# Kernel optimization log

Hardware: AMD Instinct MI355X
Metric: run time of the kernel (lower is better)

## Reference

```python
import jax, jax.numpy as jnp
import numpy as np
import math

B, T, N, DIN, DOUT, K, ED, H = 16, 12, 2048, 1, 64, 3, 10, 4
HORIZON, ODIM = 12, 1


def _pos_encoding(L, d, dtype):
    pos = jnp.arange(L, dtype=dtype)[:, None]
    div = jnp.exp(jnp.arange(0, d, 2, dtype=dtype) * (-math.log(10000.0) / d))
    pe = jnp.zeros((L, d), dtype)
    pe = pe.at[:, 0::2].set(jnp.sin(pos * div))
    pe = pe.at[:, 1::2].set(jnp.cos(pos * div))
    return pe  # [L, d]


def _cheb_supports(emb, cheb_k):
    # adaptive adjacency from node embeddings + Chebyshev polynomials
    A = jax.nn.softmax(jax.nn.relu(emb @ emb.T), axis=1)  # [N, N]
    supports = [jnp.eye(emb.shape[0], dtype=emb.dtype), A]
    for _ in range(2, cheb_k):
        supports.append(2.0 * (A @ supports[-1]) - supports[-2])
    return jnp.stack(supports[:cheb_k], axis=0)  # [K, N, N]


def _forward(source, targets, node_embeddings, gate_w, gate_b, update_w, update_b,
             attn_in_w, attn_in_b, attn_out_w, attn_out_b, channel_w, conv_w, conv_b):
    supports = _cheb_supports(node_embeddings, K)  # [K, N, N]
    # per-node adaptive weights (hoisted out of the time loop: constant per step)
    gw = jnp.einsum('nd,dkio->nkio', node_embeddings, gate_w)    # [N,K,DIN+DOUT,2*DOUT]
    gb = node_embeddings @ gate_b                                 # [N,2*DOUT]
    uw = jnp.einsum('nd,dkio->nkio', node_embeddings, update_w)  # [N,K,DIN+DOUT,DOUT]
    ub = node_embeddings @ update_b                               # [N,DOUT]

    def gconv(x, w, b):  # x: [B,N,C]
        xg = jnp.einsum('knm,bmc->bnkc', supports, x)
        return jnp.einsum('bnki,nkio->bno', xg, w) + b

    def gru(x, h):  # AGCRN GRU cell with adaptive graph conv
        ih = jnp.concatenate([x, h], axis=-1)
        zr = jax.nn.sigmoid(gconv(ih, gw, gb))
        z, r = zr[..., :DOUT], zr[..., DOUT:]
        hc = jnp.tanh(gconv(jnp.concatenate([x, z * h], axis=-1), uw, ub))
        return r * h + (1.0 - r) * hc

    h0 = jnp.zeros((B, N, DOUT), source.dtype)

    def step(carry, xt):
        s, ls = carry
        s2, ls2 = gru(xt, s), gru(xt, ls)
        return (s2, ls2), (s2, ls2)

    xs = jnp.swapaxes(source, 0, 1)  # [T,B,N,DIN]
    _, (states, last_states) = jax.lax.scan(step, (h0, h0), xs)
    states = jnp.swapaxes(states, 0, 1)            # [B,T,N,DOUT]
    last_states = jnp.swapaxes(last_states, 0, 1)  # [B,T,N,DOUT]

    # TransformerLayer applied to pass-1 states (eval: dropout is identity)
    def transformer(X):
        Bx, Tx, Nx, E = X.shape
        Xf = jnp.swapaxes(X, 0, 1).reshape(Tx, Bx * Nx, E)
        Xf = Xf + _pos_encoding(Tx, E, X.dtype)[:, None, :]
        qkv = Xf @ attn_in_w.T + attn_in_b
        q, k, v = jnp.split(qkv, 3, axis=-1)
        hd = E // H
        q = q.reshape(Tx, Bx * Nx, H, hd)
        k = k.reshape(Tx, Bx * Nx, H, hd)
        v = v.reshape(Tx, Bx * Nx, H, hd)
        scores = jnp.einsum('tmhd,smhd->mhts', q, k) / jnp.sqrt(jnp.asarray(hd, X.dtype))
        attn = jax.nn.softmax(scores, axis=-1)
        out = jnp.einsum('mhts,smhd->tmhd', attn, v).reshape(Tx, Bx * Nx, E)
        out = out @ attn_out_w.T + attn_out_b
        return jnp.swapaxes(out.reshape(Tx, Bx, Nx, E), 0, 1)

    current_inputs = transformer(states)   # pass 1 (with transformer)
    current_inputs_short = states          # pass 2 recomputes identical recurrence
    current_last_inputs = last_states

    o1 = current_inputs[:, -1]        # [B,N,DOUT]
    o2 = current_last_inputs[:, -1]
    o3 = current_inputs_short[:, -1]
    feat = jnp.stack([o1, o2, o3], axis=1)            # [B,3,N,DOUT]
    feat = feat * channel_w[None, :, None, None]
    out = jnp.einsum('bcnh,och->bon', feat, conv_w) + conv_b[None, :, None]  # [B,H*O,N]
    out = out.reshape(B, HORIZON, ODIM, N).transpose(0, 1, 3, 2)             # [B,H,N,O]
    return out


def setup_inputs() -> dict:
    key = jax.random.key(0)
    ks = jax.random.split(key, 10)
    s = 0.05
    return dict(
        source=jax.random.normal(ks[0], (B, T, N, DIN), jnp.float32),
        targets=jax.random.normal(ks[1], (B, HORIZON, N, ODIM), jnp.float32),
        node_embeddings=jax.random.normal(ks[2], (N, ED), jnp.float32),
        gate_w=jax.random.normal(ks[3], (ED, K, DIN + DOUT, 2 * DOUT), jnp.float32) * s,
        gate_b=jax.random.normal(ks[4], (ED, 2 * DOUT), jnp.float32) * s,
        update_w=jax.random.normal(ks[5], (ED, K, DIN + DOUT, DOUT), jnp.float32) * s,
        update_b=jax.random.normal(ks[6], (ED, DOUT), jnp.float32) * s,
        attn_in_w=jax.random.normal(ks[7], (3 * DOUT, DOUT), jnp.float32) * s,
        attn_in_b=jnp.zeros((3 * DOUT,), jnp.float32),
        attn_out_w=jax.random.normal(ks[8], (DOUT, DOUT), jnp.float32) * s,
        attn_out_b=jnp.zeros((DOUT,), jnp.float32),
        channel_w=jnp.ones((3,), jnp.float32),
        conv_w=jax.random.normal(ks[9], (HORIZON * ODIM, 3, DOUT), jnp.float32) * s,
        conv_b=jnp.zeros((HORIZON * ODIM,), jnp.float32),
    )


def reference(source, targets, node_embeddings, gate_w, gate_b, update_w, update_b,
              attn_in_w, attn_in_b, attn_out_w, attn_out_b, channel_w, conv_w, conv_b):
    return _forward(source, targets, node_embeddings, gate_w, gate_b, update_w, update_b,
                    attn_in_w, attn_in_b, attn_out_w, attn_out_b, channel_w, conv_w, conv_b)
```

## Files before the change

kernel.cpp:

```cpp
#include <hip/hip_runtime.h>
#include <hip/hip_bf16.h>

typedef _Float16 f16x8 __attribute__((ext_vector_type(8)));
typedef _Float16 f16x4 __attribute__((ext_vector_type(4)));
typedef float f32x4 __attribute__((ext_vector_type(4)));
typedef unsigned short us8 __attribute__((ext_vector_type(8)));
typedef unsigned short us4 __attribute__((ext_vector_type(4)));

#define N_ 2048
#define B_ 16
#define T_ 12
#define DH 64
#define CC 65
#define NC 1040
#define NCP 1088
#define KI 195
#define NKC 25
#define EDIM 10
#define ASCALE 1024.0f
#define AINV (1.0f / 1024.0f)

__global__ __launch_bounds__(256) void k_compA(const float* __restrict__ emb,
                                               _Float16* __restrict__ A) {
    int n = blockIdx.x, tid = threadIdx.x;
    float en[EDIM];
#pragma unroll
    for (int d = 0; d < EDIM; ++d) en[d] = emb[n * EDIM + d];
    float v[8], mx = -1e30f;
#pragma unroll
    for (int j = 0; j < 8; ++j) {
        int m = tid + j * 256;
        float acc = 0.f;
#pragma unroll
        for (int d = 0; d < EDIM; ++d) acc = fmaf(en[d], emb[m * EDIM + d], acc);
        acc = fmaxf(acc, 0.f);
        v[j] = acc; mx = fmaxf(mx, acc);
    }
    __shared__ float red[256];
    red[tid] = mx; __syncthreads();
    for (int s = 128; s > 0; s >>= 1) { if (tid < s) red[tid] = fmaxf(red[tid], red[tid + s]); __syncthreads(); }
    mx = red[0]; __syncthreads();
    float se = 0.f;
#pragma unroll
    for (int j = 0; j < 8; ++j) { v[j] = __expf(v[j] - mx); se += v[j]; }
    red[tid] = se; __syncthreads();
    for (int s = 128; s > 0; s >>= 1) { if (tid < s) red[tid] += red[tid + s]; __syncthreads(); }
    float inv = ASCALE / red[0];
#pragma unroll
    for (int j = 0; j < 8; ++j) A[(long)n * N_ + tid + j * 256] = (_Float16)(v[j] * inv);
}

__global__ __launch_bounds__(256) void k_transp(const _Float16* __restrict__ A,
                                                _Float16* __restrict__ AT) {
    __shared__ _Float16 tile[64][72];
    int bx = blockIdx.x, by = blockIdx.y;
    int tid = threadIdx.x;
    int r8 = tid >> 3, c8 = (tid & 7) * 8;
#pragma unroll
    for (int p = 0; p < 2; ++p) {
        int r = p * 32 + r8;
        *(f16x8*)&tile[r][c8] = *(const f16x8*)(A + (long)(by * 64 + r) * N_ + bx * 64 + c8);
    }
    __syncthreads();
#pragma unroll
    for (int p = 0; p < 2; ++p) {
        int r = p * 32 + r8;
        f16x8 v;
#pragma unroll
        for (int q = 0; q < 8; ++q) v[q] = tile[c8 + q][r];
        *(f16x8*)(AT + (long)(bx * 64 + r) * N_ + by * 64 + c8) = v;
    }
}

__global__ __launch_bounds__(256) void k_build(const float* __restrict__ emb,
        const float* __restrict__ gw, const float* __restrict__ gb,
        const float* __restrict__ uw, const float* __restrict__ ub,
        _Float16* __restrict__ GwT, float* __restrict__ Gb,
        _Float16* __restrict__ UwT, float* __restrict__ Ub) {
    int bid = blockIdx.x;
    int tid = threadIdx.x;
    if (bid < 800) {
        __shared__ float embs[128][EDIM];
        int isupd = bid >= 400;
        int b2 = isupd ? bid - 400 : bid;
        int kkc = b2 >> 4, nch = b2 & 15;
        for (int idx = tid; idx < 128 * EDIM; idx += 256)
            embs[idx / EDIM][idx % EDIM] = emb[(nch * 128 + idx / EDIM) * EDIM + idx % EDIM];
        __syncthreads();
        if (!isupd) {
            int o = tid >> 1, jh = (tid & 1) * 4;
            float w[EDIM][4];
#pragma unroll
            for (int d = 0; d < EDIM; ++d)
#pragma unroll
                for (int jj = 0; jj < 4; ++jj) {
                    int kk = kkc * 8 + jh + jj;
                    w[d][jj] = (kk < KI) ? gw[(long)d * (KI * 128) + (long)kk * 128 + o] : 0.f;
                }
            for (int i = 0; i < 128; ++i) {
                int n = nch * 128 + i;
                float a0 = 0.f, a1 = 0.f, a2 = 0.f, a3 = 0.f;
#pragma unroll
                for (int d = 0; d < EDIM; ++d) {
                    float ed = embs[i][d];
                    a0 = fmaf(ed, w[d][0], a0); a1 = fmaf(ed, w[d][1], a1);
                    a2 = fmaf(ed, w[d][2], a2); a3 = fmaf(ed, w[d][3], a3);
                }
                us4 pk;
                pk[0] = __builtin_bit_cast(unsigned short, (_Float16)a0);
                pk[1] = __builtin_bit_cast(unsigned short, (_Float16)a1);
                pk[2] = __builtin_bit_cast(unsigned short, (_Float16)a2);
                pk[3] = __builtin_bit_cast(unsigned short, (_Float16)a3);
                *(us4*)(GwT + ((long)n * NKC + kkc) * 1024 + o * 8 + jh) = pk;
            }
        } else {
            int sub = tid >> 7, o = (tid >> 1) & 63, jh = (tid & 1) * 4;
            float w[EDIM][4];
#pragma unroll
            for (int d = 0; d < EDIM; ++d)
#pragma unroll
                for (int jj = 0; jj < 4; ++jj) {
                    int kk = kkc * 8 + jh + jj;
                    w[d][jj] = (kk < KI) ? uw[(long)d * (KI * 64) + (long)kk * 64 + o] : 0.f;
                }
            for (int i = 0; i < 64; ++i) {
                int il = i * 2 + sub;
                int n = nch * 128 + il;
                float a0 = 0.f, a1 = 0.f, a2 = 0.f, a3 = 0.f;
#pragma unroll
                for (int d = 0; d < EDIM; ++d) {
                    float ed = embs[il][d];
                    a0 = fmaf(ed, w[d][0], a0); a1 = fmaf(ed, w[d][1], a1);
                    a2 = fmaf(ed, w[d][2], a2); a3 = fmaf(ed, w[d][3], a3);
                }
                us4 pk;
                pk[0] = __builtin_bit_cast(unsigned short, (_Float16)a0);
                pk[1] = __builtin_bit_cast(unsigned short, (_Float16)a1);
                pk[2] = __builtin_bit_cast(unsigned short, (_Float16)a2);
                pk[3] = __builtin_bit_cast(unsigned short, (_Float16)a3);
                *(us4*)(UwT + ((long)n * NKC + kkc) * 512 + o * 8 + jh) = pk;
            }
        }
    } else {
        int bb = bid - 800;
        const int CHUNK = (2048 * 128 + 2048 * 64) / 16;
        for (int idx = bb * CHUNK + tid; idx < (bb + 1) * CHUNK; idx += 256) {
            if (idx < 2048 * 128) {
                int n = idx >> 7, o = idx & 127;
                float a = 0.f;
#pragma unroll
                for (int d = 0; d < EDIM; ++d) a = fmaf(emb[n * EDIM + d], gb[d * 128 + o], a);
                Gb[idx] = a;
            } else {
                int i2 = idx - 2048 * 128;
                int n = i2 >> 6, o = i2 & 63;
                float a = 0.f;
#pragma unroll
                for (int d = 0; d < EDIM; ++d) a = fmaf(emb[n * EDIM + d], ub[d * 64 + o], a);
                Ub[i2] = a;
            }
        }
    }
}

__global__ __launch_bounds__(256) void k_wcvt(const float* __restrict__ Wi,
        const float* __restrict__ Wo, _Float16* __restrict__ Wi16,
        _Float16* __restrict__ Wo16) {
    int idx = blockIdx.x * 256 + threadIdx.x;
    if (idx < 192 * 64) Wi16[idx] = (_Float16)Wi[idx];
    if (idx < 64 * 64) Wo16[idx] = (_Float16)Wo[idx];
}

__global__ __launch_bounds__(256) void k_initx(const float* __restrict__ src,
        _Float16* __restrict__ XT) {
    int idx = blockIdx.x * 256 + threadIdx.x;
    int b = idx >> 11, n = idx & 2047;
    XT[((long)b * CC) * N_ + n] = (_Float16)src[((long)b * T_) * N_ + n];
}

__device__ __forceinline__ f16x8 lds_frag(const _Float16* base, int r, int kb) {
    int byt = r * 128 + ((kb * 2) ^ ((r & 7) << 4));
    return *(const f16x8*)((const char*)base + byt);
}

__device__ __forceinline__ void gemm_body(const _Float16* __restrict__ Aop,
        const _Float16* __restrict__ BT, _Float16* __restrict__ DT,
        int bm, int bc, int tid, _Float16* As, _Float16* Bs) {
    int wid = tid >> 6, lane = tid & 63;
    int row_g = bm * 64, col_g = bc * 64;
    int r0 = (wid & 1) * 32, c0 = (wid >> 1) * 32;

    int lr8 = lane >> 3;
    int lsw = 8 * ((lane & 7) ^ lr8);
    long aoff[2], boff[2];
    int ldo[2];
#pragma unroll
    for (int i = 0; i < 2; ++i) {
        aoff[i] = (long)(row_g + wid * 16 + i * 8 + lr8) * N_ + lsw;
        boff[i] = (long)(col_g + wid * 16 + i * 8 + lr8) * N_ + lsw;
        ldo[i] = (wid * 16 + i * 8) * 64;
    }
    auto stage = [&](int buf, int kt) {
        int k0 = kt * 64;
#pragma unroll
        for (int i = 0; i < 2; ++i)
            __builtin_amdgcn_global_load_lds(
                (const __attribute__((address_space(1))) void*)(Aop + aoff[i] + k0),
                (__attribute__((address_space(3))) void*)&As[buf * 4096 + ldo[i]], 16, 0, 0);
#pragma unroll
        for (int i = 0; i < 2; ++i)
            __builtin_amdgcn_global_load_lds(
                (const __attribute__((address_space(1))) void*)(BT + boff[i] + k0),
                (__attribute__((address_space(3))) void*)&Bs[buf * 4096 + ldo[i]], 16, 0, 0);
    };

    f32x4 acc[2][2] = {};
    const int NT = 32;
    stage(0, 0);
    stage(1, 1);
    int buf = 0;
    for (int kt = 0; kt < NT; ++kt) {
        if (kt + 2 < NT) {
            stage((buf + 2) % 3, kt + 2);
            asm volatile("s_waitcnt vmcnt(8)" ::: "memory");
        } else if (kt + 1 < NT) {
            asm volatile("s_waitcnt vmcnt(4)" ::: "memory");
        } else {
            asm volatile("s_waitcnt vmcnt(0)" ::: "memory");
        }
        __builtin_amdgcn_s_barrier();
        const _Float16* Ab = As + buf * 4096;
        const _Float16* Bb = Bs + buf * 4096;
#pragma unroll
        for (int kk = 0; kk < 64; kk += 32) {
            int kb = kk + (lane >> 4) * 8;
            f16x8 af0 = lds_frag(Ab, r0 + (lane & 15), kb);
            f16x8 af1 = lds_frag(Ab, r0 + 16 + (lane & 15), kb);
            f16x8 bf0 = lds_frag(Bb, c0 + (lane & 15), kb);
            f16x8 bf1 = lds_frag(Bb, c0 + 16 + (lane & 15), kb);
            acc[0][0] = __builtin_amdgcn_mfma_f32_16x16x32_f16(af0, bf0, acc[0][0], 0, 0, 0);
            acc[0][1] = __builtin_amdgcn_mfma_f32_16x16x32_f16(af0, bf1, acc[0][1], 0, 0, 0);
            acc[1][0] = __builtin_amdgcn_mfma_f32_16x16x32_f16(af1, bf0, acc[1][0], 0, 0, 0);
            acc[1][1] = __builtin_amdgcn_mfma_f32_16x16x32_f16(af1, bf1, acc[1][1], 0, 0, 0);
        }
        asm volatile("s_waitcnt lgkmcnt(0)" ::: "memory");
        __builtin_amdgcn_s_barrier();
        buf = (buf + 1) % 3;
    }
#pragma unroll
    for (int rt = 0; rt < 2; ++rt)
#pragma unroll
        for (int ct = 0; ct < 2; ++ct) {
            int cg = col_g + c0 + ct * 16 + (lane & 15);
            int ng = row_g + r0 + rt * 16 + ((lane >> 4) << 2);
            us4 pk;
#pragma unroll
            for (int q = 0; q < 4; ++q) pk[q] = __builtin_bit_cast(unsigned short, (_Float16)(acc[rt][ct][q] * AINV));
            *(us4*)(DT + (long)cg * N_ + ng) = pk;
        }
}

__global__ __launch_bounds__(256) void k_gemm(const _Float16* __restrict__ Aop,
        const _Float16* __restrict__ BT, _Float16* __restrict__ DT) {
    __shared__ __align__(16) _Float16 As[3 * 64 * 64];
    __shared__ __align__(16) _Float16 Bs[3 * 64 * 64];
    gemm_body(Aop, BT, DT, blockIdx.x, blockIdx.y, threadIdx.x, As, Bs);
}

__global__ __launch_bounds__(256) void k_gemm2(const _Float16* __restrict__ A,
        const _Float16* __restrict__ A2, const _Float16* __restrict__ BT,
        _Float16* __restrict__ Y1T, _Float16* __restrict__ Y2T) {
    __shared__ __align__(16) _Float16 As[3 * 64 * 64];
    __shared__ __align__(16) _Float16 Bs[3 * 64 * 64];
    const _Float16* Aop = blockIdx.z ? A2 : A;
    _Float16* DT = blockIdx.z ? Y2T : Y1T;
    gemm_body(Aop, BT, DT, blockIdx.x, blockIdx.y, threadIdx.x, As, Bs);
}

__global__ __launch_bounds__(256) void k_apply_gate(const float* __restrict__ src,
        const _Float16* __restrict__ h, const _Float16* __restrict__ Y1T,
        const _Float16* __restrict__ Y2T, const _Float16* __restrict__ GwT,
        const float* __restrict__ Gb, int t,
        _Float16* __restrict__ z, _Float16* __restrict__ r, _Float16* __restrict__ XT,
        const _Float16* __restrict__ zp) {
    int n = blockIdx.x, tid = threadIdx.x, wid = tid >> 6, lane = tid & 63;
    __shared__ __align__(16) _Float16 xg[16][232];
    _Float16* xf = &xg[0][0];
    for (int idx = tid; idx < 16 * 232; idx += 256) xf[idx] = (_Float16)0.f;
    __syncthreads();
    for (int idx = tid; idx < 16 * KI; idx += 256) {
        int b = idx / KI, kk = idx % KI;
        int k = kk / CC, i = kk % CC;
        float ih = (i == 0) ? src[((long)b * T_ + t) * N_ + n]
                            : (float)h[((long)b * N_ + n) * DH + (i - 1)];
        float val;
        if (k == 0)      val = ih;
        else if (k == 1) val = (float)Y1T[(long)(b * CC + i) * N_ + n];
        else             val = 2.f * (float)Y2T[(long)(b * CC + i) * N_ + n] - ih;
        xg[b][kk] = (_Float16)val;
    }
    __syncthreads();
    const _Float16* Wp = GwT + (long)n * (NKC * 128 * 8);
    int cl = lane & 15, q = lane >> 4, k8 = q * 8;
    int o0 = wid * 32 + cl, o1 = o0 + 16;
    f32x4 acc0 = {}, acc1 = {};
#pragma unroll
    for (int ks = 0; ks < 7; ++ks) {
        f16x8 af = *(const f16x8*)&xg[cl][ks * 32 + k8];
        bool valid = (ks * 4 + q) < NKC;
        const _Float16* p0 = valid ? Wp + (long)((ks * 4 + q) * 128 + o0) * 8 : zp + cl * 8;
        const _Float16* p1 = valid ? Wp + (long)((ks * 4 + q) * 128 + o1) * 8 : zp + cl * 8 + 128;
        f16x8 b0 = *(const f16x8*)p0;
        f16x8 b1 = *(const f16x8*)p1;
        acc0 = __builtin_amdgcn_mfma_f32_16x16x32_f16(af, b0, acc0, 0, 0, 0);
        acc1 = __builtin_amdgcn_mfma_f32_16x16x32_f16(af, b1, acc1, 0, 0, 0);
    }
#pragma unroll
    for (int tl = 0; tl < 2; ++tl) {
        f32x4 acc = tl ? acc1 : acc0;
        int o = wid * 32 + tl * 16 + cl;
        float bias = Gb[(long)n * 128 + o];
#pragma unroll
        for (int qq = 0; qq < 4; ++qq) {
            int b = q * 4 + qq;
            float sv = 1.f / (1.f + __expf(-(acc[qq] + bias)));
            long base = ((long)b * N_ + n) * DH;
            if (o < 64) {
                z[base + o] = (_Float16)sv;
                XT[(long)(b * CC + 1 + o) * N_ + n] = (_Float16)(sv * (float)h[base + o]);
            } else {
                r[base + (o - 64)] = (_Float16)sv;
            }
        }
    }
}

__global__ __launch_bounds__(256) void k_apply_update(const float* __restrict__ src,
        _Float16* __restrict__ h, const _Float16* __restrict__ Y1T,
        const _Float16* __restrict__ Y2T, const _Float16* __restrict__ UwT,
        const float* __restrict__ Ub, const _Float16* __restrict__ z,
        const _Float16* __restrict__ rb, int t, _Float16* __restrict__ states,
        _Float16* __restrict__ XT, const _Float16* __restrict__ zp) {
    int n = blockIdx.x, tid = threadIdx.x, wid = tid >> 6, lane = tid & 63;
    __shared__ __align__(16) _Float16 xg[16][232];
    _Float16* xf = &xg[0][0];
    for (int idx = tid; idx < 16 * 232; idx += 256) xf[idx] = (_Float16)0.f;
    __syncthreads();
    for (int idx = tid; idx < 16 * KI; idx += 256) {
        int b = idx / KI, kk = idx % KI;
        int k = kk / CC, i = kk % CC;
        float ih;
        if (i == 0) ih = src[((long)b * T_ + t) * N_ + n];
        else {
            long base = ((long)b * N_ + n) * DH + (i - 1);
            ih = (float)h[base] * (float)z[base];
        }
        float val;
        if (k == 0)      val = ih;
        else if (k == 1) val = (float)Y1T[(long)(b * CC + i) * N_ + n];
        else             val = 2.f * (float)Y2T[(long)(b * CC + i) * N_ + n] - ih;
        xg[b][kk] = (_Float16)val;
    }
    __syncthreads();
    const _Float16* Wp = UwT + (long)n * (NKC * 64 * 8);
    int cl = lane & 15, q = lane >> 4, k8 = q * 8;
    int o0 = wid * 16 + cl;
    f32x4 acc0 = {};
#pragma unroll
    for (int ks = 0; ks < 7; ++ks) {
        f16x8 af = *(const f16x8*)&xg[cl][ks * 32 + k8];
        bool valid = (ks * 4 + q) < NKC;
        const _Float16* p0 = valid ? Wp + (long)((ks * 4 + q) * 64 + o0) * 8 : zp + cl * 8;
        f16x8 b0 = *(const f16x8*)p0;
        acc0 = __builtin_amdgcn_mfma_f32_16x16x32_f16(af, b0, acc0, 0, 0, 0);
    }
    int o = o0;
    float bias = Ub[(long)n * 64 + o];
#pragma unroll
    for (int qq = 0; qq < 4; ++qq) {
        int b = q * 4 + qq;
        long base = ((long)b * N_ + n) * DH + o;
        float hc = tanhf(acc0[qq] + bias);
        float rv = (float)rb[base], hv = (float)h[base];
        float hn = rv * hv + (1.f - rv) * hc;
        _Float16 hn16 = (_Float16)hn;
        h[base] = hn16;
        states[(((long)b * T_ + t) * N_ + n) * DH + o] = hn16;
        XT[(long)(b * CC + 1 + o) * N_ + n] = hn16;
        if (o == 0 && t + 1 < T_)
            XT[(long)(b * CC) * N_ + n] = (_Float16)src[((long)b * T_ + t + 1) * N_ + n];
    }
}

__global__ __launch_bounds__(256) void k_qkv(const _Float16* __restrict__ st,
        const _Float16* __restrict__ Wi16, const float* __restrict__ bi,
        _Float16* __restrict__ KV, _Float16* __restrict__ Q) {
    int bt = blockIdx.x;
    int nck = blockIdx.y;
    int b = bt / 12, t = bt % 12;
    int tid = threadIdx.x, wid = tid >> 6, lane = tid & 63;
    __shared__ float pe[64];
    __shared__ __align__(16) _Float16 Xs[128][72];
    if (tid < 64) {
        int e = tid;
        float div = __powf(10000.f, -(float)(e & ~1) / 64.f);
        float ang = (float)t * div;
        pe[e] = (e & 1) ? __cosf(ang) : __sinf(ang);
    }
    __syncthreads();
    const _Float16* srcp = st + ((long)(b * T_ + t) * N_ + nck * 128) * DH;
#pragma unroll
    for (int u = 0; u < 4; ++u) {
        int idx = u * 256 + tid;
        int rr = idx >> 3, e0 = (idx & 7) * 8;
        f16x8 v = *(const f16x8*)(srcp + rr * DH + e0);
        f16x8 ov;
#pragma unroll
        for (int q = 0; q < 8; ++q) ov[q] = (_Float16)((float)v[q] + pe[e0 + q]);
        *(f16x8*)&Xs[rr][e0] = ov;
    }
    __syncthreads();
    int cl = lane & 15, ks8 = (lane >> 4) * 8;
    f16x8 bfrag[3][2];
    float bias[3];
#pragma unroll
    for (int j = 0; j < 3; ++j) {
        int c = (wid * 3 + j) * 16 + cl;
#pragma unroll
        for (int ks = 0; ks < 2; ++ks)
            bfrag[j][ks] = *(const f16x8*)(Wi16 + c * 64 + ks * 32 + ks8);
        bias[j] = bi[c];
    }
    f32x4 acc[8][3] = {};
#pragma unroll
    for (int rt = 0; rt < 8; ++rt) {
#pragma unroll
        for (int ks = 0; ks < 2; ++ks) {
            f16x8 af = *(const f16x8*)&Xs[rt * 16 + cl][ks * 32 + ks8];
#pragma unroll
            for (int j = 0; j < 3; ++j)
                acc[rt][j] = __builtin_amdgcn_mfma_f32_16x16x32_f16(af, bfrag[j][ks], acc[rt][j], 0, 0, 0);
        }
    }
    int rowq = (lane >> 4) * 4;
#pragma unroll
    for (int rt = 0; rt < 8; ++rt)
#pragma unroll
        for (int j = 0; j < 3; ++j) {
            int c = (wid * 3 + j) * 16 + cl;
#pragma unroll
            for (int q = 0; q < 4; ++q) {
                int n = nck * 128 + rt * 16 + rowq + q;
                float val = acc[rt][j][q] + bias[j];
                if (c >= 64)
                    KV[(((long)b * N_ + n) * T_ + t) * 128 + (c - 64)] = (_Float16)val;
                else if (t == 11)
                    Q[((long)b * N_ + n) * 64 + c] = (_Float16)val;
            }
        }
}

__global__ __launch_bounds__(256) void k_attn2(const _Float16* __restrict__ KV,
        const _Float16* __restrict__ Q, const _Float16* __restrict__ Wo16,
        const float* __restrict__ bo, float* __restrict__ o1) {
    __shared__ _Float16 kvs[16 * 1544];
    __shared__ float qs[16][64];
    __shared__ float Wos[64][64];
    __shared__ float outb[16][64];
    __shared__ float bos[64];
    int tid = threadIdx.x;
    long pair0 = (long)blockIdx.x * 16;
#pragma unroll
    for (int u = 0; u < 12; ++u) {
        int idx = u * 256 + tid;
        int p = idx / 192, off8 = (idx % 192) * 8;
        *(f16x8*)&kvs[p * 1544 + off8] = *(const f16x8*)(KV + (pair0 + p) * 1536 + off8);
    }
    if (tid < 64) bos[tid] = bo[tid];
    for (int idx = tid; idx < 1024; idx += 256) {
        int p = idx >> 6, j = idx & 63;
        qs[p][j] = (float)Q[(pair0 + p) * 64 + j];
    }
    for (int idx = tid; idx < 4096; idx += 256) {
        int c = idx >> 6, j = idx & 63;
        Wos[c][j] = (float)Wo16[j * 64 + c];
    }
    __syncthreads();
    int p = tid >> 4, i = tid & 15;
    int h = i >> 2, sg = i & 3;
    const _Float16* kvp = &kvs[p * 1544];
    float att3[3], mx = -1e30f;
#pragma unroll
    for (int j = 0; j < 3; ++j) {
        int s = sg + 4 * j;
        float sc = 0.f;
#pragma unroll
        for (int d = 0; d < 16; ++d)
            sc = fmaf(qs[p][h * 16 + d], (float)kvp[s * 128 + h * 16 + d], sc);
        att3[j] = sc * 0.25f;
        mx = fmaxf(mx, att3[j]);
    }
    mx = fmaxf(mx, __shfl_xor(mx, 1));
    mx = fmaxf(mx, __shfl_xor(mx, 2));
    float se = 0.f;
#pragma unroll
    for (int j = 0; j < 3; ++j) { att3[j] = __expf(att3[j] - mx); se += att3[j]; }
    se += __shfl_xor(se, 1);
    se += __shfl_xor(se, 2);
    float inv = 1.f / se;
#pragma unroll
    for (int j = 0; j < 3; ++j) att3[j] *= inv;
    int c0 = i * 4;
    float out4[4] = {0.f, 0.f, 0.f, 0.f};
#pragma unroll
    for (int m = 0; m < 4; ++m) {
        float a0 = __shfl_xor(att3[0], m);
        float a1 = __shfl_xor(att3[1], m);
        float a2 = __shfl_xor(att3[2], m);
        int sb = sg ^ m;
        float aj[3] = {a0, a1, a2};
#pragma unroll
        for (int j = 0; j < 3; ++j) {
            int s = sb + 4 * j;
            f16x4 vv = *(const f16x4*)&kvp[s * 128 + 64 + c0];
#pragma unroll
            for (int q = 0; q < 4; ++q) out4[q] = fmaf(aj[j], (float)vv[q], out4[q]);
        }
    }
    *(float4*)&outb[p][c0] = *(float4*)out4;
    __syncthreads();
    float res[4];
#pragma unroll
    for (int q = 0; q < 4; ++q) res[q] = bos[c0 + q];
    for (int c = 0; c < 64; ++c) {
        float oc = outb[p][c];
        float4 wv = *(const float4*)&Wos[c][c0];
        res[0] = fmaf(oc, wv.x, res[0]);
        res[1] = fmaf(oc, wv.y, res[1]);
        res[2] = fmaf(oc, wv.z, res[2]);
        res[3] = fmaf(oc, wv.w, res[3]);
    }
    *(float4*)&o1[(pair0 + p) * 64 + c0] = make_float4(res[0], res[1], res[2], res[3]);
}

__global__ __launch_bounds__(256) void k_final(const float* __restrict__ o1,
        const _Float16* __restrict__ hT, const float* __restrict__ cw,
        const float* __restrict__ convw, const float* __restrict__ convb,
        float* __restrict__ out) {
    __shared__ float Ws[12 * 3 * 64];
    __shared__ float cbs[12];
    int tid = threadIdx.x;
    for (int idx = tid; idx < 12 * 3 * 64; idx += 256) Ws[idx] = convw[idx];
    if (tid < 12) cbs[tid] = convb[tid];
    __syncthreads();
    float c0 = cw[0], c1 = cw[1], c2 = cw[2];
    int g = tid >> 6, j = tid & 63;
    int bn = blockIdx.x * 4 + g;
    int b = bn >> 11, n = bn & 2047;
    float x1 = o1[(long)bn * DH + j];
    float x3 = (float)hT[(long)bn * DH + j];
    float myout = 0.f;
#pragma unroll
    for (int oc = 0; oc < 12; ++oc) {
        float p = x1 * c0 * Ws[(oc * 3 + 0) * 64 + j]
                + x3 * (c1 * Ws[(oc * 3 + 1) * 64 + j] + c2 * Ws[(oc * 3 + 2) * 64 + j]);
        p += __shfl_xor(p, 1); p += __shfl_xor(p, 2); p += __shfl_xor(p, 4);
        p += __shfl_xor(p, 8); p += __shfl_xor(p, 16); p += __shfl_xor(p, 32);
        if (j == oc) myout = p + cbs[oc];
    }
    if (j < 12) out[((long)b * 12 + j) * N_ + n] = myout;
}

extern "C" void kernel_launch(void* const* d_in, const int* in_sizes, int n_in,
                              void* d_out, int out_size, void* d_ws, size_t ws_size,
                              hipStream_t stream) {
    const float* src    = (const float*)d_in[0];
    const float* emb    = (const float*)d_in[2];
    const float* gate_w = (const float*)d_in[3];
    const float* gate_b = (const float*)d_in[4];
    const float* upd_w  = (const float*)d_in[5];
    const float* upd_b  = (const float*)d_in[6];
    const float* a_in_w = (const float*)d_in[7];
    const float* a_in_b = (const float*)d_in[8];
    const float* a_out_w= (const float*)d_in[9];
    const float* a_out_b= (const float*)d_in[10];
    const float* chan_w = (const float*)d_in[11];
    const float* conv_w = (const float*)d_in[12];
    const float* conv_b = (const float*)d_in[13];
    float* out = (float*)d_out;

    char* ws = (char*)d_ws;
    size_t off = 0;
    auto alloc = [&](size_t bytes) { char* p = ws + off; off += (bytes + 255) & ~size_t(255); return p; };
    _Float16* A    = (_Float16*)alloc((size_t)N_ * N_ * 2);
    _Float16* A2   = (_Float16*)alloc((size_t)N_ * N_ * 2);
    _Float16* GwT  = (_Float16*)alloc((size_t)N_ * NKC * 128 * 8 * 2);
    float*  Gb     = (float*) alloc((size_t)N_ * 128 * 4);
    _Float16* UwT  = (_Float16*)alloc((size_t)N_ * NKC * 64 * 8 * 2);
    float*  Ub     = (float*) alloc((size_t)N_ * 64 * 4);
    _Float16* XT   = (_Float16*)alloc((size_t)NCP * N_ * 2);
    _Float16* Y1T  = (_Float16*)alloc((size_t)NCP * N_ * 2);
    _Float16* Y2T  = (_Float16*)alloc((size_t)NCP * N_ * 2);
    _Float16* h    = (_Float16*)alloc((size_t)B_ * N_ * DH * 2);
    _Float16* zbuf = (_Float16*)alloc((size_t)B_ * N_ * DH * 2);
    _Float16* rbuf = (_Float16*)alloc((size_t)B_ * N_ * DH * 2);
    _Float16* stt  = (_Float16*)alloc((size_t)B_ * T_ * N_ * DH * 2);
    _Float16* Wi16 = (_Float16*)alloc(192 * 64 * 2);
    _Float16* Wo16 = (_Float16*)alloc(64 * 64 * 2);
    _Float16* zp   = (_Float16*)alloc(512);
    if (off > ws_size) return;

    _Float16* AT = stt;
    _Float16* KV = GwT;
    _Float16* Qb = UwT;
    float*    o1 = (float*)((char*)UwT + (8u << 20));

    hipMemsetAsync(h, 0, (size_t)B_ * N_ * DH * 2, stream);
    hipMemsetAsync(XT, 0, (size_t)NCP * N_ * 2, stream);
    hipMemsetAsync(zp, 0, 512, stream);
    k_compA<<<N_, 256, 0, stream>>>(emb, A);
    dim3 tgrid(32, 32);
    k_transp<<<tgrid, 256, 0, stream>>>(A, AT);
    k_gemm<<<tgrid, 256, 0, stream>>>(AT, A, A2);
    k_build<<<816, 256, 0, stream>>>(emb, gate_w, gate_b, upd_w, upd_b, GwT, Gb, UwT, Ub);
    k_wcvt<<<48, 256, 0, stream>>>(a_in_w, a_out_w, Wi16, Wo16);
    k_initx<<<128, 256, 0, stream>>>(src, XT);

    dim3 ggrid(32, 17, 2);
    for (int t = 0; t < T_; ++t) {
        k_gemm2<<<ggrid, 256, 0, stream>>>(A, A2, XT, Y1T, Y2T);
        k_apply_gate<<<N_, 256, 0, stream>>>(src, h, Y1T, Y2T, GwT, Gb, t, zbuf, rbuf, XT, zp);
        k_gemm2<<<ggrid, 256, 0, stream>>>(A, A2, XT, Y1T, Y2T);
        k_apply_update<<<N_, 256, 0, stream>>>(src, h, Y1T, Y2T, UwT, Ub, zbuf, rbuf, t, stt, XT, zp);
    }
    dim3 qgrid(192, 16);
    k_qkv<<<qgrid, 256, 0, stream>>>(stt, Wi16, a_in_b, KV, Qb);
    k_attn2<<<2048, 256, 0, stream>>>(KV, Qb, Wo16, a_out_b, o1);
    k_final<<<8192, 256, 0, stream>>>(o1, h, chan_w, conv_w, conv_b, out);
}
```

Baseline: 2.365 ms.

## Fuse A and A2 graph GEMMs to share B tiles; prefetch per-node weights

The two support GEMMs (A·X and A2·X) now run in one kernel that stages the shared XT tile once per k-step and computes both products, instead of a z=2 grid that loaded XT twice. This halves the B-operand traffic and removes one block dimension, but leaves only 544 blocks per launch and raises LDS use to 72KB per block, which may reduce occupancy. Separately, the gate and update kernels issue their per-node weight loads into registers before building the LDS tile, so global latency overlaps the gather work at the cost of more registers.

```diff
diff --git a/kernel.cpp b/kernel.cpp
--- a/kernel.cpp
+++ b/kernel.cpp
@@ -183,13 +183,14 @@
     return *(const f16x8*)((const char*)base + byt);
 }
 
-__device__ __forceinline__ void gemm_body(const _Float16* __restrict__ Aop,
-        const _Float16* __restrict__ BT, _Float16* __restrict__ DT,
-        int bm, int bc, int tid, _Float16* As, _Float16* Bs) {
+__global__ __launch_bounds__(256) void k_gemm(const _Float16* __restrict__ Aop,
+        const _Float16* __restrict__ BT, _Float16* __restrict__ DT) {
+    __shared__ __align__(16) _Float16 As[3 * 4096];
+    __shared__ __align__(16) _Float16 Bs[3 * 4096];
+    int bm = blockIdx.x, bc = blockIdx.y, tid = threadIdx.x;
     int wid = tid >> 6, lane = tid & 63;
     int row_g = bm * 64, col_g = bc * 64;
     int r0 = (wid & 1) * 32, c0 = (wid >> 1) * 32;
-
     int lr8 = lane >> 3;
     int lsw = 8 * ((lane & 7) ^ lr8);
     long aoff[2], boff[2];
@@ -213,21 +214,14 @@
                 (const __attribute__((address_space(1))) void*)(BT + boff[i] + k0),
                 (__attribute__((address_space(3))) void*)&Bs[buf * 4096 + ldo[i]], 16, 0, 0);
     };
-
     f32x4 acc[2][2] = {};
     const int NT = 32;
-    stage(0, 0);
-    stage(1, 1);
+    stage(0, 0); stage(1, 1);
     int buf = 0;
     for (int kt = 0; kt < NT; ++kt) {
-        if (kt + 2 < NT) {
-            stage((buf + 2) % 3, kt + 2);
-            asm volatile("s_waitcnt vmcnt(8)" ::: "memory");
-        } else if (kt + 1 < NT) {
-            asm volatile("s_waitcnt vmcnt(4)" ::: "memory");
-        } else {
-            asm volatile("s_waitcnt vmcnt(0)" ::: "memory");
-        }
+        if (kt + 2 < NT) { stage((buf + 2) % 3, kt + 2); asm volatile("s_waitcnt vmcnt(8)" ::: "memory"); }
+        else if (kt + 1 < NT) { asm volatile("s_waitcnt vmcnt(4)" ::: "memory"); }
+        else { asm volatile("s_waitcnt vmcnt(0)" ::: "memory"); }
         __builtin_amdgcn_s_barrier();
         const _Float16* Ab = As + buf * 4096;
         const _Float16* Bb = Bs + buf * 4096;
@@ -260,21 +254,93 @@
         }
 }
 
-__global__ __launch_bounds__(256) void k_gemm(const _Float16* __restrict__ Aop,
-        const _Float16* __restrict__ BT, _Float16* __restrict__ DT) {
-    __shared__ __align__(16) _Float16 As[3 * 64 * 64];
-    __shared__ __align__(16) _Float16 Bs[3 * 64 * 64];
-    gemm_body(Aop, BT, DT, blockIdx.x, blockIdx.y, threadIdx.x, As, Bs);
-}
-
-__global__ __launch_bounds__(256) void k_gemm2(const _Float16* __restrict__ A,
+__global__ __launch_bounds__(256) void k_gemm3(const _Float16* __restrict__ A,
         const _Float16* __restrict__ A2, const _Float16* __restrict__ BT,
         _Float16* __restrict__ Y1T, _Float16* __restrict__ Y2T) {
-    __shared__ __align__(16) _Float16 As[3 * 64 * 64];
-    __shared__ __align__(16) _Float16 Bs[3 * 64 * 64];
-    const _Float16* Aop = blockIdx.z ? A2 : A;
-    _Float16* DT = blockIdx.z ? Y2T : Y1T;
-    gemm_body(Aop, BT, DT, blockIdx.x, blockIdx.y, threadIdx.x, As, Bs);
+    __shared__ __align__(16) _Float16 As[3 * 4096];
+    __shared__ __align__(16) _Float16 A2s[3 * 4096];
+    __shared__ __align__(16) _Float16 Bs[3 * 4096];
+    int bm = blockIdx.x, bc = blockIdx.y, tid = threadIdx.x;
+    int wid = tid >> 6, lane = tid & 63;
+    int row_g = bm * 64, col_g = bc * 64;
+    int r0 = (wid & 1) * 32, c0 = (wid >> 1) * 32;
+    int lr8 = lane >> 3;
+    int lsw = 8 * ((lane & 7) ^ lr8);
+    long aoff[2], boff[2];
+    int ldo[2];
+#pragma unroll
+    for (int i = 0; i < 2; ++i) {
+        aoff[i] = (long)(row_g + wid * 16 + i * 8 + lr8) * N_ + lsw;
+        boff[i] = (long)(col_g + wid * 16 + i * 8 + lr8) * N_ + lsw;
+        ldo[i] = (wid * 16 + i * 8) * 64;
+    }
+    auto stage = [&](int buf, int kt) {
+        int k0 = kt * 64;
+#pragma unroll
+        for (int i = 0; i < 2; ++i)
+            __builtin_amdgcn_global_load_lds(
+                (const __attribute__((address_space(1))) void*)(A + aoff[i] + k0),
+                (__attribute__((address_space(3))) void*)&As[buf * 4096 + ldo[i]], 16, 0, 0);
+#pragma unroll
+        for (int i = 0; i < 2; ++i)
+            __builtin_amdgcn_global_load_lds(
+                (const __attribute__((address_space(1))) void*)(A2 + aoff[i] + k0),
+                (__attribute__((address_space(3))) void*)&A2s[buf * 4096 + ldo[i]], 16, 0, 0);
+#pragma unroll
+        for (int i = 0; i < 2; ++i)
+            __builtin_amdgcn_global_load_lds(
+                (const __attribute__((address_space(1))) void*)(BT + boff[i] + k0),
+                (__attribute__((address_space(3))) void*)&Bs[buf * 4096 + ldo[i]], 16, 0, 0);
+    };
+    f32x4 acc[2][2] = {}, acc2[2][2] = {};
+    const int NT = 32;
+    stage(0, 0); stage(1, 1);
+    int buf = 0;
+    for (int kt = 0; kt < NT; ++kt) {
+        if (kt + 2 < NT) { stage((buf + 2) % 3, kt + 2); asm volatile("s_waitcnt vmcnt(12)" ::: "memory"); }
+        else if (kt + 1 < NT) { asm volatile("s_waitcnt vmcnt(6)" ::: "memory"); }
+        else { asm volatile("s_waitcnt vmcnt(0)" ::: "memory"); }
+        __builtin_amdgcn_s_barrier();
+        const _Float16* Ab = As + buf * 4096;
+        const _Float16* A2b = A2s + buf * 4096;
+        const _Float16* Bb = Bs + buf * 4096;
+#pragma unroll
+        for (int kk = 0; kk < 64; kk += 32) {
+            int kb = kk + (lane >> 4) * 8;
+            f16x8 bf0 = lds_frag(Bb, c0 + (lane & 15), kb);
+            f16x8 bf1 = lds_frag(Bb, c0 + 16 + (lane & 15), kb);
+            f16x8 af0 = lds_frag(Ab, r0 + (lane & 15), kb);
+            f16x8 af1 = lds_frag(Ab, r0 + 16 + (lane & 15), kb);
+            f16x8 gf0 = lds_frag(A2b, r0 + (lane & 15), kb);
+            f16x8 gf1 = lds_frag(A2b, r0 + 16 + (lane & 15), kb);
+            acc[0][0] = __builtin_amdgcn_mfma_f32_16x16x32_f16(af0, bf0, acc[0][0], 0, 0, 0);
+            acc[0][1] = __builtin_amdgcn_mfma_f32_16x16x32_f16(af0, bf1, acc[0][1], 0, 0, 0);
+            acc[1][0] = __builtin_amdgcn_mfma_f32_16x16x32_f16(af1, bf0, acc[1][0], 0, 0, 0);
+            acc[1][1] = __builtin_amdgcn_mfma_f32_16x16x32_f16(af1, bf1, acc[1][1], 0, 0, 0);
+            acc2[0][0] = __builtin_amdgcn_mfma_f32_16x16x32_f16(gf0, bf0, acc2[0][0], 0, 0, 0);
+            acc2[0][1] = __builtin_amdgcn_mfma_f32_16x16x32_f16(gf0, bf1, acc2[0][1], 0, 0, 0);
+            acc2[1][0] = __builtin_amdgcn_mfma_f32_16x16x32_f16(gf1, bf0, acc2[1][0], 0, 0, 0);
+            acc2[1][1] = __builtin_amdgcn_mfma_f32_16x16x32_f16(gf1, bf1, acc2[1][1], 0, 0, 0);
+        }
+        asm volatile("s_waitcnt lgkmcnt(0)" ::: "memory");
+        __builtin_amdgcn_s_barrier();
+        buf = (buf + 1) % 3;
+    }
+#pragma unroll
+    for (int rt = 0; rt < 2; ++rt)
+#pragma unroll
+        for (int ct = 0; ct < 2; ++ct) {
+            int cg = col_g + c0 + ct * 16 + (lane & 15);
+            int ng = row_g + r0 + rt * 16 + ((lane >> 4) << 2);
+            us4 pk, pk2;
+#pragma unroll
+            for (int q = 0; q < 4; ++q) {
+                pk[q]  = __builtin_bit_cast(unsigned short, (_Float16)(acc[rt][ct][q] * AINV));
+                pk2[q] = __builtin_bit_cast(unsigned short, (_Float16)(acc2[rt][ct][q] * AINV));
+            }
+            *(us4*)(Y1T + (long)cg * N_ + ng) = pk;
+            *(us4*)(Y2T + (long)cg * N_ + ng) = pk2;
+        }
 }
 
 __global__ __launch_bounds__(256) void k_apply_gate(const float* __restrict__ src,
@@ -285,6 +351,18 @@
         const _Float16* __restrict__ zp) {
     int n = blockIdx.x, tid = threadIdx.x, wid = tid >> 6, lane = tid & 63;
     __shared__ __align__(16) _Float16 xg[16][232];
+    const _Float16* Wp = GwT + (long)n * (NKC * 128 * 8);
+    int cl = lane & 15, q = lane >> 4, k8 = q * 8;
+    int o0 = wid * 32 + cl, o1 = o0 + 16;
+    f16x8 bfr0[7], bfr1[7];
+#pragma unroll
+    for (int ks = 0; ks < 7; ++ks) {
+        bool valid = (ks * 4 + q) < NKC;
+        const _Float16* p0 = valid ? Wp + (long)((ks * 4 + q) * 128 + o0) * 8 : zp + cl * 8;
+        const _Float16* p1 = valid ? Wp + (long)((ks * 4 + q) * 128 + o1) * 8 : zp + cl * 8 + 128;
+        bfr0[ks] = *(const f16x8*)p0;
+        bfr1[ks] = *(const f16x8*)p1;
+    }
     _Float16* xf = &xg[0][0];
     for (int idx = tid; idx < 16 * 232; idx += 256) xf[idx] = (_Float16)0.f;
     __syncthreads();
@@ -300,20 +378,12 @@
         xg[b][kk] = (_Float16)val;
     }
     __syncthreads();
-    const _Float16* Wp = GwT + (long)n * (NKC * 128 * 8);
-    int cl = lane & 15, q = lane >> 4, k8 = q * 8;
-    int o0 = wid * 32 + cl, o1 = o0 + 16;
     f32x4 acc0 = {}, acc1 = {};
 #pragma unroll
     for (int ks = 0; ks < 7; ++ks) {
         f16x8 af = *(const f16x8*)&xg[cl][ks * 32 + k8];
-        bool valid = (ks * 4 + q) < NKC;
-        const _Float16* p0 = valid ? Wp + (long)((ks * 4 + q) * 128 + o0) * 8 : zp + cl * 8;
-        const _Float16* p1 = valid ? Wp + (long)((ks * 4 + q) * 128 + o1) * 8 : zp + cl * 8 + 128;
-        f16x8 b0 = *(const f16x8*)p0;
-        f16x8 b1 = *(const f16x8*)p1;
-        acc0 = __builtin_amdgcn_mfma_f32_16x16x32_f16(af, b0, acc0, 0, 0, 0);
-        acc1 = __builtin_amdgcn_mfma_f32_16x16x32_f16(af, b1, acc1, 0, 0, 0);
+        acc0 = __builtin_amdgcn_mfma_f32_16x16x32_f16(af, bfr0[ks], acc0, 0, 0, 0);
+        acc1 = __builtin_amdgcn_mfma_f32_16x16x32_f16(af, bfr1[ks], acc1, 0, 0, 0);
     }
 #pragma unroll
     for (int tl = 0; tl < 2; ++tl) {
@@ -343,6 +413,16 @@
         _Float16* __restrict__ XT, const _Float16* __restrict__ zp) {
     int n = blockIdx.x, tid = threadIdx.x, wid = tid >> 6, lane = tid & 63;
     __shared__ __align__(16) _Float16 xg[16][232];
+    const _Float16* Wp = UwT + (long)n * (NKC * 64 * 8);
+    int cl = lane & 15, q = lane >> 4, k8 = q * 8;
+    int o0 = wid * 16 + cl;
+    f16x8 bfr[7];
+#pragma unroll
+    for (int ks = 0; ks < 7; ++ks) {
+        bool valid = (ks * 4 + q) < NKC;
+        const _Float16* p0 = valid ? Wp + (long)((ks * 4 + q) * 64 + o0) * 8 : zp + cl * 8;
+        bfr[ks] = *(const f16x8*)p0;
+    }
     _Float16* xf = &xg[0][0];
     for (int idx = tid; idx < 16 * 232; idx += 256) xf[idx] = (_Float16)0.f;
     __syncthreads();
@@ -362,17 +442,11 @@
         xg[b][kk] = (_Float16)val;
     }
     __syncthreads();
-    const _Float16* Wp = UwT + (long)n * (NKC * 64 * 8);
-    int cl = lane & 15, q = lane >> 4, k8 = q * 8;
-    int o0 = wid * 16 + cl;
     f32x4 acc0 = {};
 #pragma unroll
     for (int ks = 0; ks < 7; ++ks) {
         f16x8 af = *(const f16x8*)&xg[cl][ks * 32 + k8];
-        bool valid = (ks * 4 + q) < NKC;
-        const _Float16* p0 = valid ? Wp + (long)((ks * 4 + q) * 64 + o0) * 8 : zp + cl * 8;
-        f16x8 b0 = *(const f16x8*)p0;
-        acc0 = __builtin_amdgcn_mfma_f32_16x16x32_f16(af, b0, acc0, 0, 0, 0);
+        acc0 = __builtin_amdgcn_mfma_f32_16x16x32_f16(af, bfr[ks], acc0, 0, 0, 0);
     }
     int o = o0;
     float bias = Ub[(long)n * 64 + o];
@@ -626,11 +700,11 @@
     k_wcvt<<<48, 256, 0, stream>>>(a_in_w, a_out_w, Wi16, Wo16);
     k_initx<<<128, 256, 0, stream>>>(src, XT);
 
-    dim3 ggrid(32, 17, 2);
+    dim3 ggrid(32, 17);
     for (int t = 0; t < T_; ++t) {
-        k_gemm2<<<ggrid, 256, 0, stream>>>(A, A2, XT, Y1T, Y2T);
+        k_gemm3<<<ggrid, 256, 0, stream>>>(A, A2, XT, Y1T, Y2T);
         k_apply_gate<<<N_, 256, 0, stream>>>(src, h, Y1T, Y2T, GwT, Gb, t, zbuf, rbuf, XT, zp);
-        k_gemm2<<<ggrid, 256, 0, stream>>>(A, A2, XT, Y1T, Y2T);
+        k_gemm3<<<ggrid, 256, 0, stream>>>(A, A2, XT, Y1T, Y2T);
         k_apply_update<<<N_, 256, 0, stream>>>(src, h, Y1T, Y2T, UwT, Ub, zbuf, rbuf, t, stt, XT, zp);
     }
     dim3 qgrid(192, 16);
```

Measured after the change: 2.746 ms. 16.1% more time.
